# Performance work log

Hardware: AMD Instinct MI355X
Metric: run time of the kernel (lower is better)

The kernel has to match this reference:

```python
import jax, jax.numpy as jnp
import numpy as np

T = 1_048_576          # sequence length
NUM_INPUTS = 16        # symbol vocab for _delta table
MAX_OUTPUT = 25        # softmax width / counter range


def setup_inputs() -> dict:
    key = jax.random.key(0)
    k1, k2, k3 = jax.random.split(key, 3)
    input_seq = jax.random.randint(k1, (T,), 0, NUM_INPUTS)
    # learned params (random instead of the degenerate zero init so the
    # recurrence and softmax are non-trivial)
    delta = jax.random.normal(k2, (NUM_INPUTS,), dtype=jnp.float32) * 0.5
    out_bias = jax.random.normal(k3, (MAX_OUTPUT,), dtype=jnp.float32) * 0.1
    out_scale = jnp.ones((1,), dtype=jnp.float32)
    return {"input_seq": input_seq, "delta": delta,
            "out_bias": out_bias, "out_scale": out_scale}


def reference(input_seq, delta, out_bias, out_scale):
    max_out = out_bias.shape[0]
    # per-step increments: vectorized gather  [T]
    deltas = delta[input_seq]

    # scalar counter recurrence with clamp (non-associative -> lax.scan)
    def step(c, d):
        c = jnp.clip(c + d, 0.0, float(max_out - 1))
        return c, c

    _, counters = jax.lax.scan(step, jnp.float32(0.0), deltas)  # [T]

    # vectorized readout: distances [T, max_out] -> logits -> softmax
    positions = jnp.arange(max_out, dtype=jnp.float32)
    distances = jnp.abs(positions[None, :] - counters[:, None])
    logits = -distances * out_scale + out_bias
    return jax.nn.softmax(logits, axis=-1)  # [T, max_out]
```

## Files before the change

kernel.cpp:

```cpp
#include <hip/hip_runtime.h>

#define T_LEN      1048576
#define TILE_ROWS  1024
#define NTILES     (T_LEN / TILE_ROWS)
#define MAXO       25
#define CLAMP_HI   24.0f
#define BIGF       1e30f

struct Trip { float a, l, h; };

__device__ __forceinline__ Trip comb(Trip x, Trip y) {
    Trip r;
    r.a = x.a + y.a;
    r.l = fmaxf(x.l + y.a, y.l);
    r.h = fminf(fmaxf(x.h + y.a, y.l), y.h);
    return r;
}
__device__ __forceinline__ float applyT(Trip p, float c) {
    return fminf(fmaxf(c + p.a, p.l), p.h);
}
__device__ __forceinline__ Trip shflUpTrip(Trip v, int off) {
    Trip r;
    r.a = __shfl_up(v.a, off, 64);
    r.l = __shfl_up(v.l, off, 64);
    r.h = __shfl_up(v.h, off, 64);
    return r;
}

__global__ __launch_bounds__(256)
void k1_tile(const int* __restrict__ seq, const float* __restrict__ delta,
             float* __restrict__ tri) {
    __shared__ float dl[16];
    __shared__ Trip agg[4];
    const int tid = threadIdx.x, lane = tid & 63, wid = tid >> 6;
    if (tid < 16) dl[tid] = delta[tid];
    __syncthreads();

    const int4 s4 = *(const int4*)(seq + blockIdx.x * TILE_ROWS + tid * 4);
    Trip t = {dl[s4.x], 0.0f, CLAMP_HI};
    { Trip e = {dl[s4.y], 0.0f, CLAMP_HI}; t = comb(t, e); }
    { Trip e = {dl[s4.z], 0.0f, CLAMP_HI}; t = comb(t, e); }
    { Trip e = {dl[s4.w], 0.0f, CLAMP_HI}; t = comb(t, e); }

#pragma unroll
    for (int off = 1; off < 64; off <<= 1) {
        Trip o = shflUpTrip(t, off);
        if (lane >= off) t = comb(o, t);
    }
    if (lane == 63) agg[wid] = t;
    __syncthreads();

    if (tid == 0) {
        const Trip P = comb(comb(agg[0], agg[1]), comb(agg[2], agg[3]));
        tri[3 * blockIdx.x + 0] = P.a;
        tri[3 * blockIdx.x + 1] = P.l;
        tri[3 * blockIdx.x + 2] = P.h;
    }
}

__global__ __launch_bounds__(256)
void k2_out(const int* __restrict__ seq, const float* __restrict__ delta,
            const float* __restrict__ bias, const float* __restrict__ scale,
            const float* __restrict__ tri, float* __restrict__ out) {
    __shared__ float tile[256 * MAXO];
    __shared__ float c_arr[TILE_ROWS];
    __shared__ Trip  agg[4], agg2[4];
    __shared__ float dl[16], bs[MAXO];

    const int tid = threadIdx.x, lane = tid & 63, wid = tid >> 6;
    const int bid = blockIdx.x;

    if (tid < 16)   dl[tid] = delta[tid];
    if (tid < MAXO) bs[tid] = bias[tid];
    const float sfac = scale[0];

    const int4 s4 = *(const int4*)(seq + bid * TILE_ROWS + tid * 4);
    const float4* p = (const float4*)(tri + tid * 12);
    const float4 f0 = p[0], f1 = p[1], f2 = p[2];
    __syncthreads();

    const Trip ID = {0.0f, -BIGF, BIGF};
    const int base = tid * 4;
    Trip g0 = (base + 0 < bid) ? Trip{f0.x, f0.y, f0.z} : ID;
    Trip g1 = (base + 1 < bid) ? Trip{f0.w, f1.x, f1.y} : ID;
    Trip g2 = (base + 2 < bid) ? Trip{f1.z, f1.w, f2.x} : ID;
    Trip g3 = (base + 3 < bid) ? Trip{f2.y, f2.z, f2.w} : ID;
    Trip ginc = comb(comb(g0, g1), comb(g2, g3));
#pragma unroll
    for (int off = 1; off < 64; off <<= 1) {
        Trip o = shflUpTrip(ginc, off);
        if (lane >= off) ginc = comb(o, ginc);
    }
    if (lane == 63) agg2[wid] = ginc;

    const Trip t0 = {dl[s4.x], 0.0f, CLAMP_HI};
    const Trip t1 = {dl[s4.y], 0.0f, CLAMP_HI};
    const Trip t2 = {dl[s4.z], 0.0f, CLAMP_HI};
    const Trip t3 = {dl[s4.w], 0.0f, CLAMP_HI};
    Trip inc = comb(comb(t0, t1), comb(t2, t3));
#pragma unroll
    for (int off = 1; off < 64; off <<= 1) {
        Trip o = shflUpTrip(inc, off);
        if (lane >= off) inc = comb(o, inc);
    }
    if (lane == 63) agg[wid] = inc;
    __syncthreads();

    const Trip E = comb(comb(agg2[0], agg2[1]), comb(agg2[2], agg2[3]));

    float cb = applyT(E, 0.0f);
    for (int w = 0; w < wid; ++w) cb = applyT(agg[w], cb);
    const Trip prev = shflUpTrip(inc, 1);
    const float c_in = (lane == 0) ? cb : applyT(prev, cb);
    float4 cv;
    cv.x = applyT(t0, c_in);
    cv.y = applyT(t1, cv.x);
    cv.z = applyT(t2, cv.y);
    cv.w = applyT(t3, cv.z);
    *(float4*)(c_arr + 4 * tid) = cv;
    __syncthreads();

    const size_t outbase = (size_t)bid * TILE_ROWS * MAXO;
#pragma unroll 1
    for (int r = 0; r < 4; ++r) {
        const float c = c_arr[r * 256 + tid];
        float ev[MAXO];
        float sum = 0.0f;
#pragma unroll
        for (int j = 0; j < MAXO; ++j) {
            ev[j] = __expf(fmaf(-sfac, fabsf((float)j - c), bs[j]));
            sum += ev[j];
        }
        const float rinv = 1.0f / sum;
#pragma unroll
        for (int j = 0; j < MAXO; ++j)
            tile[tid * MAXO + j] = ev[j] * rinv;

        const float4* tp4 = (const float4*)(tile + wid * 64 * MAXO);
        float4* op4 = (float4*)(out + outbase + (size_t)(r * 256 + wid * 64) * MAXO);
#pragma unroll
        for (int k = 0; k < 7; ++k) {
            const int idx = lane + k * 64;
            if (idx < 400) op4[idx] = tp4[idx];
        }
    }
}

extern "C" void kernel_launch(void* const* d_in, const int* in_sizes, int n_in,
                              void* d_out, int out_size, void* d_ws, size_t ws_size,
                              hipStream_t stream) {
    const int*   seq   = (const int*)d_in[0];
    const float* delta = (const float*)d_in[1];
    const float* bias  = (const float*)d_in[2];
    const float* scale = (const float*)d_in[3];
    float* out = (float*)d_out;

    float* tri = (float*)d_ws;

    k1_tile<<<NTILES, 256, 0, stream>>>(seq, delta, tri);
    k2_out <<<NTILES, 256, 0, stream>>>(seq, delta, bias, scale, tri, out);
}
```

Measured before the change: 120.8 us.

## Fuse tile-reduce and output kernels with a grid-wide atomic barrier

Merges the two kernels into one. Each block publishes its tile triple, increments a global counter and spins until all 1024 blocks have arrived, then computes the carry-in and the softmax output. This removes a kernel launch and the second read of the sequence, at the cost of an extra memset launch and a grid barrier that assumes all 1024 blocks are co-resident (4 per CU with about 30KB of LDS each). A bounded spin guard prevents an infinite hang but could yield wrong results if co-residency fails.

```diff
diff --git a/kernel.cpp b/kernel.cpp
--- a/kernel.cpp
+++ b/kernel.cpp
@@ -28,40 +28,11 @@
 }
 
 __global__ __launch_bounds__(256)
-void k1_tile(const int* __restrict__ seq, const float* __restrict__ delta,
-             float* __restrict__ tri) {
-    __shared__ float dl[16];
-    __shared__ Trip agg[4];
-    const int tid = threadIdx.x, lane = tid & 63, wid = tid >> 6;
-    if (tid < 16) dl[tid] = delta[tid];
-    __syncthreads();
-
-    const int4 s4 = *(const int4*)(seq + blockIdx.x * TILE_ROWS + tid * 4);
-    Trip t = {dl[s4.x], 0.0f, CLAMP_HI};
-    { Trip e = {dl[s4.y], 0.0f, CLAMP_HI}; t = comb(t, e); }
-    { Trip e = {dl[s4.z], 0.0f, CLAMP_HI}; t = comb(t, e); }
-    { Trip e = {dl[s4.w], 0.0f, CLAMP_HI}; t = comb(t, e); }
-
-#pragma unroll
-    for (int off = 1; off < 64; off <<= 1) {
-        Trip o = shflUpTrip(t, off);
-        if (lane >= off) t = comb(o, t);
-    }
-    if (lane == 63) agg[wid] = t;
-    __syncthreads();
-
-    if (tid == 0) {
-        const Trip P = comb(comb(agg[0], agg[1]), comb(agg[2], agg[3]));
-        tri[3 * blockIdx.x + 0] = P.a;
-        tri[3 * blockIdx.x + 1] = P.l;
-        tri[3 * blockIdx.x + 2] = P.h;
-    }
-}
-
-__global__ __launch_bounds__(256)
-void k2_out(const int* __restrict__ seq, const float* __restrict__ delta,
-            const float* __restrict__ bias, const float* __restrict__ scale,
-            const float* __restrict__ tri, float* __restrict__ out) {
+void k_fused(const int* __restrict__ seq, const float* __restrict__ delta,
+             const float* __restrict__ bias, const float* __restrict__ scale,
+             unsigned* __restrict__ ctr, float* __restrict__ tri,
+             float* __restrict__ out)
+{
     __shared__ float tile[256 * MAXO];
     __shared__ float c_arr[TILE_ROWS];
     __shared__ Trip  agg[4], agg2[4];
@@ -75,10 +46,41 @@
     const float sfac = scale[0];
 
     const int4 s4 = *(const int4*)(seq + bid * TILE_ROWS + tid * 4);
+    __syncthreads();
+
+    const Trip t0 = {dl[s4.x], 0.0f, CLAMP_HI};
+    const Trip t1 = {dl[s4.y], 0.0f, CLAMP_HI};
+    const Trip t2 = {dl[s4.z], 0.0f, CLAMP_HI};
+    const Trip t3 = {dl[s4.w], 0.0f, CLAMP_HI};
+    Trip inc = comb(comb(t0, t1), comb(t2, t3));
+#pragma unroll
+    for (int off = 1; off < 64; off <<= 1) {
+        Trip o = shflUpTrip(inc, off);
+        if (lane >= off) inc = comb(o, inc);
+    }
+    if (lane == 63) agg[wid] = inc;
+    __syncthreads();
+
+    if (tid == 0) {
+        const Trip P = comb(comb(agg[0], agg[1]), comb(agg[2], agg[3]));
+        tri[3 * bid + 0] = P.a;
+        tri[3 * bid + 1] = P.l;
+        tri[3 * bid + 2] = P.h;
+        __threadfence();
+        __hip_atomic_fetch_add(ctr, 1u, __ATOMIC_RELEASE,
+                               __HIP_MEMORY_SCOPE_AGENT);
+        int guard = 0;
+        while (__hip_atomic_load(ctr, __ATOMIC_ACQUIRE,
+                                 __HIP_MEMORY_SCOPE_AGENT) < NTILES) {
+            __builtin_amdgcn_s_sleep(2);
+            if (++guard >= (1 << 24)) break;
+        }
+    }
+    __syncthreads();
+    (void)__hip_atomic_load(ctr, __ATOMIC_ACQUIRE, __HIP_MEMORY_SCOPE_AGENT);
+
     const float4* p = (const float4*)(tri + tid * 12);
     const float4 f0 = p[0], f1 = p[1], f2 = p[2];
-    __syncthreads();
-
     const Trip ID = {0.0f, -BIGF, BIGF};
     const int base = tid * 4;
     Trip g0 = (base + 0 < bid) ? Trip{f0.x, f0.y, f0.z} : ID;
@@ -92,18 +94,6 @@
         if (lane >= off) ginc = comb(o, ginc);
     }
     if (lane == 63) agg2[wid] = ginc;
-
-    const Trip t0 = {dl[s4.x], 0.0f, CLAMP_HI};
-    const Trip t1 = {dl[s4.y], 0.0f, CLAMP_HI};
-    const Trip t2 = {dl[s4.z], 0.0f, CLAMP_HI};
-    const Trip t3 = {dl[s4.w], 0.0f, CLAMP_HI};
-    Trip inc = comb(comb(t0, t1), comb(t2, t3));
-#pragma unroll
-    for (int off = 1; off < 64; off <<= 1) {
-        Trip o = shflUpTrip(inc, off);
-        if (lane >= off) inc = comb(o, inc);
-    }
-    if (lane == 63) agg[wid] = inc;
     __syncthreads();
 
     const Trip E = comb(comb(agg2[0], agg2[1]), comb(agg2[2], agg2[3]));
@@ -155,8 +145,9 @@
     const float* scale = (const float*)d_in[3];
     float* out = (float*)d_out;
 
-    float* tri = (float*)d_ws;
+    unsigned* ctr = (unsigned*)d_ws;
+    float*    tri = (float*)((char*)d_ws + 256);
 
-    k1_tile<<<NTILES, 256, 0, stream>>>(seq, delta, tri);
-    k2_out <<<NTILES, 256, 0, stream>>>(seq, delta, bias, scale, tri, out);
+    hipMemsetAsync(d_ws, 0, 256, stream);
+    k_fused<<<NTILES, 256, 0, stream>>>(seq, delta, bias, scale, ctr, tri, out);
 }
```

After: 214.9 us. 78.0% more time.
